# Optimization experiments

Hardware: AMD Instinct MI355X
Metric: run time of the kernel (lower is better)

## Reference

```python
import jax, jax.numpy as jnp
import numpy as np

B, C, IN_LEN, OUT_LEN, E, TOP_K, N_I = 1, 8192, 512, 512, 8, 2, 16


def setup_inputs() -> dict:
    key = jax.random.key(0)
    ks = jax.random.split(key, 8)
    w = lambda k, shape, sc=0.02: jax.random.normal(k, shape, dtype=jnp.float32) * sc
    return {
        "x": jax.random.normal(ks[0], (B, C, IN_LEN), dtype=jnp.float32),
        "Ins_tk": jax.random.normal(ks[1], (B, N_I, OUT_LEN), dtype=jnp.float32),
        "gate_w": w(ks[2], (IN_LEN, E)),            # Gate: Linear(in_len, E, bias=False)
        "expert_w": w(ks[3], (E, IN_LEN, OUT_LEN)),  # per-expert Linear weight (transposed)
        "expert_b": jnp.zeros((E, OUT_LEN), dtype=jnp.float32),
        "gamma_w": w(ks[4], (E, OUT_LEN)),          # EiLM gamma_generator: Linear(h,1,bias=False)
        "beta_w": w(ks[5], (E, OUT_LEN, OUT_LEN)),  # EiLM beta_generator (transposed)
        "rmod_w": w(ks[6], (OUT_LEN, E)),           # router_modulator: Linear(out_len, E, bias=False)
    }


def reference(x, Ins_tk, gate_w, expert_w, expert_b, gamma_w, beta_w, rmod_w):
    Bx, Cx, L = x.shape
    xf = x.reshape(-1, L)                                   # [N, in_len], N = B*C
    ins = Ins_tk[0]                                         # [N_i, out_len] (B==1 asserted)

    # Router: logits + expert-wise modulation of logits
    router_gamma = jnp.mean(ins @ rmod_w, axis=0)           # [E]
    logits = xf @ gate_w + router_gamma                     # [N, E]
    probs = jax.nn.softmax(logits.astype(jnp.float32), axis=-1)
    rw, sel = jax.lax.top_k(probs, TOP_K)                   # [N, k] values/indices (no renorm)

    # Combine weights per token per expert: sum_k rw[t,k] * onehot(sel[t,k])
    combine = jnp.sum(jax.nn.one_hot(sel, E, dtype=rw.dtype) * rw[..., None], axis=1)  # [N, E]

    # EiLM per-expert affine params: scalar gamma, vector beta (mean over instruction tokens)
    gam = jnp.mean(ins @ gamma_w.T, axis=0)                 # [E]
    bet = jnp.einsum('nh,ehd->ed', ins, beta_w) / N_I       # [E, out_len]

    # Per-expert linear over all tokens, then EiLM modulation
    eo = jnp.einsum('nl,eld->end', xf, expert_w) + expert_b[:, None, :]   # [E, N, out]
    mod = gam[:, None, None] * eo + bet[:, None, :]                        # [E, N, out]

    out = jnp.einsum('ne,end->nd', combine, mod)            # [N, out]
    return out.reshape(Bx, Cx, OUT_LEN)
```

## Files before the change

kernel.cpp:

```cpp
#include <hip/hip_runtime.h>
#include <hip/hip_bf16.h>

#define N_TOK 8192
#define INL   512
#define OUTL  512
#define NE    8
#define NI    16
#define EOFF  (OUTL * INL)

typedef unsigned short ushort_t;
typedef unsigned int   uint_t;
typedef short  short8  __attribute__((ext_vector_type(8)));
typedef float  floatx4 __attribute__((ext_vector_type(4)));

#define WS_CNT    0u
#define WS_GAM    4096u
#define WS_RGAM   4352u
#define WS_SCHED  4608u
#define WS_BET    8192u
#define WS_SELW   32768u
#define WS_WT     163840u
#define WS_LIST   4358144u
#define MAXTP     184

__device__ __forceinline__ ushort_t f2bf(float f) {
    uint_t b = __float_as_uint(f);
    return (ushort_t)((b + 0x7FFFu + ((b >> 16) & 1u)) >> 16);
}
__device__ __forceinline__ uint_t pkbf(float a, float b) {
    __hip_bfloat162 h = __float22bfloat162_rn(make_float2(a, b));
    union { __hip_bfloat162 h2; uint_t u; } cv;
    cv.h2 = h;
    return cv.u;
}
__device__ __forceinline__ void dma16(const ushort_t* g, ushort_t* l) {
    __builtin_amdgcn_global_load_lds(
        (const __attribute__((address_space(1))) void*)g,
        (__attribute__((address_space(3))) void*)l,
        16, 0, 0);
}

__global__ __launch_bounds__(256)
void k_prep(const float* __restrict__ ins,
            const float* __restrict__ expert_w,
            const float* __restrict__ expert_b,
            const float* __restrict__ gamma_w,
            const float* __restrict__ beta_w,
            const float* __restrict__ rmod_w,
            ushort_t* __restrict__ wt,
            float* __restrict__ wsBet,
            float* __restrict__ wsGam, float* __restrict__ wsRgam,
            int* __restrict__ wsCnt) {
    __shared__ __align__(16) char smem[17152];
    int bx = blockIdx.x;
    int tid = threadIdx.x;

    if (bx < 512) {
        float (*tile)[65] = (float(*)[65])smem;
        int e = bx >> 6, rem = bx & 63;
        int lt = (rem >> 3) * 64, dt = (rem & 7) * 64;
        int dIdx = tid & 63, lq = tid >> 6;
        for (int i = 0; i < 16; ++i) {
            int l = lq * 16 + i;
            tile[l][dIdx] = expert_w[(e * INL + lt + l) * OUTL + dt + dIdx];
        }
        __syncthreads();
        int lIdx = tid & 63, dq = tid >> 6;
        for (int i = 0; i < 16; ++i) {
            int d = dq * 16 + i;
            wt[(e * OUTL + dt + d) * INL + lt + lIdx] = f2bf(tile[lIdx][d]);
        }
        return;
    }

    if (bx < 640) {
        float* sS  = (float*)smem;
        float* red = sS + 512;
        float* gamS = red + 256;
        int b2 = bx - 512;
        int e = b2 >> 4, dBase = (b2 & 15) * 32;
        for (int h = tid; h < INL; h += 256) {
            float a = 0.f;
            for (int n = 0; n < NI; ++n) a += ins[n * INL + h];
            sS[h] = a;
        }
        __syncthreads();
        if (tid < 64) {
            float g = 0.f;
            for (int j = 0; j < 8; ++j) g += sS[tid * 8 + j] * gamma_w[e * INL + tid * 8 + j];
            for (int off = 32; off >= 1; off >>= 1) g += __shfl_xor(g, off, 64);
            if (tid == 0) gamS[0] = g * (1.f / NI);
        }
        int doff = tid & 31, hq = tid >> 5;
        float a = 0.f;
        for (int j = 0; j < 64; ++j) {
            int h = hq * 64 + j;
            a += sS[h] * beta_w[(e * INL + h) * OUTL + dBase + doff];
        }
        red[tid] = a;
        __syncthreads();
        if (tid < 32) {
            float t = 0.f;
            for (int k = 0; k < 8; ++k) t += red[k * 32 + tid];
            int d = dBase + tid;
            wsBet[e * OUTL + d] = t * (1.f / NI) + gamS[0] * expert_b[e * OUTL + d];
        }
        return;
    }

    {
        if (tid < 64) wsCnt[tid * 16] = 0;
        float* sS = (float*)smem;
        float* pg = sS + 512;
        float* pr = pg + 64;
        for (int h = tid; h < INL; h += 256) {
            float a = 0.f;
            for (int n = 0; n < NI; ++n) a += ins[n * INL + h];
            sS[h] = a;
        }
        __syncthreads();
        if (tid < 64) {
            int e = tid & 7, qq = tid >> 3;
            float g = 0.f, r = 0.f;
            for (int j = 0; j < 64; ++j) {
                int h = qq * 64 + j;
                float sv = sS[h];
                g += sv * gamma_w[e * INL + h];
                r += sv * rmod_w[h * NE + e];
            }
            pg[tid] = g; pr[tid] = r;
        }
        __syncthreads();
        if (tid < NE) {
            float g = 0.f, r = 0.f;
            for (int qq = 0; qq < 8; ++qq) { g += pg[qq * 8 + tid]; r += pr[qq * 8 + tid]; }
            wsGam[tid]  = g * (1.f / NI);
            wsRgam[tid] = r * (1.f / NI);
        }
    }
}

__global__ __launch_bounds__(256)
void k_route(const float* __restrict__ x,
             const float* __restrict__ gate_w,
             const float* __restrict__ wsGam,
             const float* __restrict__ wsRgam,
             float4* __restrict__ selW,
             int* __restrict__ wsCnt, int* __restrict__ wsList) {
    __shared__ float gateT[NE * INL];
    __shared__ int tokP[16];
    __shared__ int cnt64[64], base64[64], pos[16];

    int tid = threadIdx.x;
    for (int i = 0; i < 16; ++i) {
        int f = tid + 256 * i;
        gateT[(f & 7) * INL + (f >> 3)] = gate_w[f];
    }
    if (tid < 64) cnt64[tid] = 0;
    __syncthreads();

    int w = tid >> 6, lane = tid & 63;
    int tbase = blockIdx.x * 16 + w * 4;

    for (int tt = 0; tt < 4; ++tt) {
        int t = tbase + tt;
        float2 xv[4];
        for (int i = 0; i < 4; ++i)
            xv[i] = *(const float2*)(x + (size_t)t * INL + 2 * lane + 128 * i);

        float acc[NE];
        for (int e = 0; e < NE; ++e) acc[e] = 0.f;
        for (int i = 0; i < 4; ++i) {
            int c = 2 * lane + 128 * i;
            for (int e = 0; e < NE; ++e)
                acc[e] += xv[i].x * gateT[e * INL + c] + xv[i].y * gateT[e * INL + c + 1];
        }
        for (int e = 0; e < NE; ++e) {
            float a = acc[e];
            for (int off = 32; off >= 1; off >>= 1) a += __shfl_xor(a, off, 64);
            acc[e] = a;
        }
        float logit[NE];
        for (int e = 0; e < NE; ++e) logit[e] = acc[e] + wsRgam[e];

        int i0 = 0; float m0 = logit[0];
        for (int e = 1; e < NE; ++e) if (logit[e] > m0) { m0 = logit[e]; i0 = e; }
        int i1 = -1; float m1 = -3.4e38f;
        for (int e = 0; e < NE; ++e) if (e != i0 && logit[e] > m1) { m1 = logit[e]; i1 = e; }

        float S = 0.f;
        for (int e = 0; e < NE; ++e) S += expf(logit[e] - m0);
        float rw0 = 1.0f / S;
        float rw1 = expf(m1 - m0) / S;

        if (lane == 0) {
            selW[t] = make_float4(rw0 * wsGam[i0], rw1 * wsGam[i1], rw0, rw1);
            tokP[w * 4 + tt] = i0 * 8 + i1;
        }
    }
    __syncthreads();

    if (tid < 16) pos[tid] = atomicAdd(&cnt64[tokP[tid]], 1);
    __syncthreads();
    if (tid < 64 && cnt64[tid] > 0)
        base64[tid] = atomicAdd(wsCnt + tid * 16, cnt64[tid]);
    __syncthreads();
    if (tid < 16) {
        int p = tokP[tid];
        wsList[(size_t)p * N_TOK + base64[p] + pos[tid]] = blockIdx.x * 16 + tid;
    }
}

__global__ __launch_bounds__(256)
void k_sched(const int* __restrict__ wsCnt, int* __restrict__ sched) {
    __shared__ int cnt[64], base[64], totS;
    int tid = threadIdx.x;
    if (tid < 64) cnt[tid] = wsCnt[tid * 16];
    __syncthreads();
    if (tid == 0) {
        int run = 0;
        for (int i = 0; i < 64; ++i) {
            base[i] = run;
            run += (cnt[i] + 63) >> 6;
        }
        totS = run;
    }
    __syncthreads();
    if (tid < 64) {
        int c = cnt[tid], ti = (c + 63) >> 6, b = base[tid];
        for (int j = 0; j < ti; ++j)
            sched[b + j] = tid | (j << 6) | (c << 14);
    }
    for (int j = totS + tid; j < MAXTP; j += 256)
        sched[j] = -1;
}

__global__ __launch_bounds__(256, 4)
void k_gemmp(const float* __restrict__ x, const ushort_t* __restrict__ wt,
             const int* __restrict__ sched, const int* __restrict__ wsList,
             const float4* __restrict__ selW, const float* __restrict__ wsBet,
             float* __restrict__ out) {
    int bx = blockIdx.x;
    int ct = bx & 7;
    int bt = bx >> 3;

    int s = sched[bt];
    if (s < 0) return;
    int li = s & 63, lt = (s >> 6) & 127, cntE = s >> 14;
    int e0 = li >> 3, e1 = li & 7;
    const int* listE = wsList + (size_t)li * N_TOK;

    __shared__ ushort_t Blds[2][2][64 * 64];

    int tid = threadIdx.x;
    int wid = tid >> 6, lane = tid & 63;
    int wm = wid * 16;
    int mrow = lane & 15, laneq = lane >> 4, q8 = laneq * 8, qr = laneq * 4;

    int idx = lt * 64 + wm + mrow;
    int tok = 0; float w0 = 0.f, w1 = 0.f;
    if (idx < cntE) {
        tok = listE[idx];
        float4 w4 = selW[tok];
        w0 = w4.x; w1 = w4.y;
    }
    const float* arowp = x + (size_t)tok * INL + q8;

    int c0 = tid;
    int col0 = c0 >> 3, kg0 = ((c0 & 7) - col0) & 7;
    const ushort_t* pB = wt + (size_t)e0 * EOFF + (size_t)(ct * 64 + col0) * INL + kg0 * 8;
    ptrdiff_t dE = (ptrdiff_t)(e1 - e0) * EOFF;
    ushort_t* ldsA = &Blds[0][0][0] + wid * 512;

    int fcol[4], frot0[4];
    for (int nt = 0; nt < 4; ++nt) {
        fcol[nt] = nt * 16 + mrow;
        frot0[nt] = (laneq + fcol[nt]) & 7;
    }

    floatx4 comb[4];
    for (int nt = 0; nt < 4; ++nt) comb[nt] = (floatx4){0.f, 0.f, 0.f, 0.f};

    dma16(pB,                 ldsA);
    dma16(pB + 32 * INL,      ldsA + 2048);
    dma16(pB + dE,            ldsA + 4096);
    dma16(pB + dE + 32 * INL, ldsA + 6144);
    float4 a00 = *(const float4*)(arowp);
    float4 a01 = *(const float4*)(arowp + 4);
    float4 a10 = *(const float4*)(arowp + 32);
    float4 a11 = *(const float4*)(arowp + 36);
    __syncthreads();

    #pragma unroll
    for (int kc = 0; kc < 8; ++kc) {
        int buf = kc & 1;
        float4 n00, n01, n10, n11;
        if (kc < 7) {
            const ushort_t* p = pB + (kc + 1) * 64;
            ushort_t* l = ldsA + (buf ^ 1) * 8192;
            dma16(p,                 l);
            dma16(p + 32 * INL,      l + 2048);
            dma16(p + dE,            l + 4096);
            dma16(p + dE + 32 * INL, l + 6144);
            const float* ap = arowp + (kc + 1) * 64;
            n00 = *(const float4*)(ap);
            n01 = *(const float4*)(ap + 4);
            n10 = *(const float4*)(ap + 32);
            n11 = *(const float4*)(ap + 36);
        }

        const ushort_t* Bb = &Blds[buf][0][0];
        #pragma unroll
        for (int e = 0; e < 2; ++e) {
            float wv = e ? w1 : w0;
            union AF { uint4 u; short8 s; } af[2];
            af[0].u.x = pkbf(a00.x * wv, a00.y * wv);
            af[0].u.y = pkbf(a00.z * wv, a00.w * wv);
            af[0].u.z = pkbf(a01.x * wv, a01.y * wv);
            af[0].u.w = pkbf(a01.z * wv, a01.w * wv);
            af[1].u.x = pkbf(a10.x * wv, a10.y * wv);
            af[1].u.y = pkbf(a10.z * wv, a10.w * wv);
            af[1].u.z = pkbf(a11.x * wv, a11.y * wv);
            af[1].u.w = pkbf(a11.z * wv, a11.w * wv);

            const ushort_t* B = Bb + e * 4096;
            short8 bf[4][2];
            #pragma unroll
            for (int nt = 0; nt < 4; ++nt) {
                int cb = fcol[nt] * 64;
                bf[nt][0] = *(const short8*)&B[cb + frot0[nt] * 8];
                bf[nt][1] = *(const short8*)&B[cb + ((frot0[nt] + 4) & 7) * 8];
            }
            #pragma unroll
            for (int ks = 0; ks < 2; ++ks)
                for (int nt = 0; nt < 4; ++nt)
                    comb[nt] = __builtin_amdgcn_mfma_f32_16x16x32_bf16(
                        af[ks].s, bf[nt][ks], comb[nt], 0, 0, 0);
        }
        __syncthreads();
        if (kc < 7) { a00 = n00; a01 = n01; a10 = n10; a11 = n11; }
    }

    #pragma unroll
    for (int ri = 0; ri < 4; ++ri) {
        int idx2 = lt * 64 + wm + qr + ri;
        if (idx2 >= cntE) continue;
        int tok2 = listE[idx2];
        float4 w4 = selW[tok2];
        float* op = out + (size_t)tok2 * OUTL + ct * 64;
        #pragma unroll
        for (int nt = 0; nt < 4; ++nt) {
            int col = ct * 64 + nt * 16 + mrow;
            float bet = w4.z * wsBet[e0 * OUTL + col] + w4.w * wsBet[e1 * OUTL + col];
            op[nt * 16 + mrow] = comb[nt][ri] + bet;
        }
    }
}

extern "C" void kernel_launch(void* const* d_in, const int* in_sizes, int n_in,
                              void* d_out, int out_size, void* d_ws, size_t ws_size,
                              hipStream_t stream) {
    const float* x        = (const float*)d_in[0];
    const float* ins      = (const float*)d_in[1];
    const float* gate_w   = (const float*)d_in[2];
    const float* expert_w = (const float*)d_in[3];
    const float* expert_b = (const float*)d_in[4];
    const float* gamma_w  = (const float*)d_in[5];
    const float* beta_w   = (const float*)d_in[6];
    const float* rmod_w   = (const float*)d_in[7];
    float* out = (float*)d_out;

    char* ws = (char*)d_ws;
    int*      wsCnt  = (int*)(ws + WS_CNT);
    float*    wsGam  = (float*)(ws + WS_GAM);
    float*    wsRgam = (float*)(ws + WS_RGAM);
    int*      wsSch  = (int*)(ws + WS_SCHED);
    float*    wsBet  = (float*)(ws + WS_BET);
    float4*   selW   = (float4*)(ws + WS_SELW);
    ushort_t* wt     = (ushort_t*)(ws + WS_WT);
    int*      wsList = (int*)(ws + WS_LIST);

    k_prep<<<641, 256, 0, stream>>>(ins, expert_w, expert_b,
                                    gamma_w, beta_w, rmod_w,
                                    wt, wsBet, wsGam, wsRgam, wsCnt);
    k_route<<<N_TOK / 16, 256, 0, stream>>>(x, gate_w, wsGam, wsRgam,
                                            selW, wsCnt, wsList);
    k_sched<<<1, 256, 0, stream>>>(wsCnt, wsSch);
    k_gemmp<<<MAXTP * 8, 256, 0, stream>>>(x, wt, wsSch, wsList,
                                           selW, wsBet, out);
}
```

Measured before the change: 139.7 us.

## Double token tile per block to 128 rows, reusing B fragments across two row groups

Each GEMM block now covers 128 tokens instead of 64: every wave handles two 16-row fragments, so each B fragment read from LDS feeds twice as many MFMAs and the expert weight DMA is amortised over more tokens. The schedule splits each expert pair's token list into 128-token tiles, and the grid shrinks to match. The x prefetch into registers is dropped, so A loads now happen inside each k-step, and the k loop is no longer unrolled. This doubles accumulator registers and leaves fewer blocks and more padding waste on partially filled tiles.

```diff
diff --git a/kernel.cpp b/kernel.cpp
--- a/kernel.cpp
+++ b/kernel.cpp
@@ -21,7 +21,7 @@
 #define WS_SELW   32768u
 #define WS_WT     163840u
 #define WS_LIST   4358144u
-#define MAXTP     184
+#define MAXT2     120
 
 __device__ __forceinline__ ushort_t f2bf(float f) {
     uint_t b = __float_as_uint(f);
@@ -221,17 +221,17 @@
         int run = 0;
         for (int i = 0; i < 64; ++i) {
             base[i] = run;
-            run += (cnt[i] + 63) >> 6;
+            run += (cnt[i] + 127) >> 7;
         }
         totS = run;
     }
     __syncthreads();
     if (tid < 64) {
-        int c = cnt[tid], ti = (c + 63) >> 6, b = base[tid];
+        int c = cnt[tid], ti = (c + 127) >> 7, b = base[tid];
         for (int j = 0; j < ti; ++j)
             sched[b + j] = tid | (j << 6) | (c << 14);
     }
-    for (int j = totS + tid; j < MAXTP; j += 256)
+    for (int j = totS + tid; j < MAXT2; j += 256)
         sched[j] = -1;
 }
 
@@ -246,7 +246,7 @@
 
     int s = sched[bt];
     if (s < 0) return;
-    int li = s & 63, lt = (s >> 6) & 127, cntE = s >> 14;
+    int li = s & 63, lt = (s >> 6) & 63, cntE = s >> 14;
     int e0 = li >> 3, e1 = li & 7;
     const int* listE = wsList + (size_t)li * N_TOK;
 
@@ -254,17 +254,23 @@
 
     int tid = threadIdx.x;
     int wid = tid >> 6, lane = tid & 63;
-    int wm = wid * 16;
+    int wm = wid * 32;
     int mrow = lane & 15, laneq = lane >> 4, q8 = laneq * 8, qr = laneq * 4;
 
-    int idx = lt * 64 + wm + mrow;
-    int tok = 0; float w0 = 0.f, w1 = 0.f;
-    if (idx < cntE) {
-        tok = listE[idx];
-        float4 w4 = selW[tok];
-        w0 = w4.x; w1 = w4.y;
-    }
-    const float* arowp = x + (size_t)tok * INL + q8;
+    const float* arowp[2];
+    float w0v[2], w1v[2];
+    #pragma unroll
+    for (int rf = 0; rf < 2; ++rf) {
+        int idx = lt * 128 + wm + rf * 16 + mrow;
+        int tok = 0; float w0 = 0.f, w1 = 0.f;
+        if (idx < cntE) {
+            tok = listE[idx];
+            float4 w4 = selW[tok];
+            w0 = w4.x; w1 = w4.y;
+        }
+        arowp[rf] = x + (size_t)tok * INL + q8;
+        w0v[rf] = w0; w1v[rf] = w1;
+    }
 
     int c0 = tid;
     int col0 = c0 >> 3, kg0 = ((c0 & 7) - col0) & 7;
@@ -278,23 +284,20 @@
         frot0[nt] = (laneq + fcol[nt]) & 7;
     }
 
-    floatx4 comb[4];
-    for (int nt = 0; nt < 4; ++nt) comb[nt] = (floatx4){0.f, 0.f, 0.f, 0.f};
+    floatx4 comb[2][4];
+    #pragma unroll
+    for (int rf = 0; rf < 2; ++rf)
+        for (int nt = 0; nt < 4; ++nt) comb[rf][nt] = (floatx4){0.f, 0.f, 0.f, 0.f};
 
     dma16(pB,                 ldsA);
     dma16(pB + 32 * INL,      ldsA + 2048);
     dma16(pB + dE,            ldsA + 4096);
     dma16(pB + dE + 32 * INL, ldsA + 6144);
-    float4 a00 = *(const float4*)(arowp);
-    float4 a01 = *(const float4*)(arowp + 4);
-    float4 a10 = *(const float4*)(arowp + 32);
-    float4 a11 = *(const float4*)(arowp + 36);
-    __syncthreads();
-
-    #pragma unroll
+    __syncthreads();
+
+    #pragma unroll 1
     for (int kc = 0; kc < 8; ++kc) {
         int buf = kc & 1;
-        float4 n00, n01, n10, n11;
         if (kc < 7) {
             const ushort_t* p = pB + (kc + 1) * 64;
             ushort_t* l = ldsA + (buf ^ 1) * 8192;
@@ -302,27 +305,21 @@
             dma16(p + 32 * INL,      l + 2048);
             dma16(p + dE,            l + 4096);
             dma16(p + dE + 32 * INL, l + 6144);
-            const float* ap = arowp + (kc + 1) * 64;
-            n00 = *(const float4*)(ap);
-            n01 = *(const float4*)(ap + 4);
-            n10 = *(const float4*)(ap + 32);
-            n11 = *(const float4*)(ap + 36);
+        }
+
+        float4 a0[2], a1[2], a2[2], a3[2];
+        #pragma unroll
+        for (int rf = 0; rf < 2; ++rf) {
+            const float* ap = arowp[rf] + kc * 64;
+            a0[rf] = *(const float4*)(ap);
+            a1[rf] = *(const float4*)(ap + 4);
+            a2[rf] = *(const float4*)(ap + 32);
+            a3[rf] = *(const float4*)(ap + 36);
         }
 
         const ushort_t* Bb = &Blds[buf][0][0];
         #pragma unroll
         for (int e = 0; e < 2; ++e) {
-            float wv = e ? w1 : w0;
-            union AF { uint4 u; short8 s; } af[2];
-            af[0].u.x = pkbf(a00.x * wv, a00.y * wv);
-            af[0].u.y = pkbf(a00.z * wv, a00.w * wv);
-            af[0].u.z = pkbf(a01.x * wv, a01.y * wv);
-            af[0].u.w = pkbf(a01.z * wv, a01.w * wv);
-            af[1].u.x = pkbf(a10.x * wv, a10.y * wv);
-            af[1].u.y = pkbf(a10.z * wv, a10.w * wv);
-            af[1].u.z = pkbf(a11.x * wv, a11.y * wv);
-            af[1].u.w = pkbf(a11.z * wv, a11.w * wv);
-
             const ushort_t* B = Bb + e * 4096;
             short8 bf[4][2];
             #pragma unroll
@@ -331,30 +328,44 @@
                 bf[nt][0] = *(const short8*)&B[cb + frot0[nt] * 8];
                 bf[nt][1] = *(const short8*)&B[cb + ((frot0[nt] + 4) & 7) * 8];
             }
+            union AF { uint4 u; short8 s; } af[2][2];
+            #pragma unroll
+            for (int rf = 0; rf < 2; ++rf) {
+                float wv = e ? w1v[rf] : w0v[rf];
+                af[rf][0].u.x = pkbf(a0[rf].x * wv, a0[rf].y * wv);
+                af[rf][0].u.y = pkbf(a0[rf].z * wv, a0[rf].w * wv);
+                af[rf][0].u.z = pkbf(a1[rf].x * wv, a1[rf].y * wv);
+                af[rf][0].u.w = pkbf(a1[rf].z * wv, a1[rf].w * wv);
+                af[rf][1].u.x = pkbf(a2[rf].x * wv, a2[rf].y * wv);
+                af[rf][1].u.y = pkbf(a2[rf].z * wv, a2[rf].w * wv);
+                af[rf][1].u.z = pkbf(a3[rf].x * wv, a3[rf].y * wv);
+                af[rf][1].u.w = pkbf(a3[rf].z * wv, a3[rf].w * wv);
+            }
             #pragma unroll
             for (int ks = 0; ks < 2; ++ks)
-                for (int nt = 0; nt < 4; ++nt)
-                    comb[nt] = __builtin_amdgcn_mfma_f32_16x16x32_bf16(
-                        af[ks].s, bf[nt][ks], comb[nt], 0, 0, 0);
-        }
-        __syncthreads();
-        if (kc < 7) { a00 = n00; a01 = n01; a10 = n10; a11 = n11; }
+                for (int rf = 0; rf < 2; ++rf)
+                    for (int nt = 0; nt < 4; ++nt)
+                        comb[rf][nt] = __builtin_amdgcn_mfma_f32_16x16x32_bf16(
+                            af[rf][ks].s, bf[nt][ks], comb[rf][nt], 0, 0, 0);
+        }
+        __syncthreads();
     }
 
     #pragma unroll
-    for (int ri = 0; ri < 4; ++ri) {
-        int idx2 = lt * 64 + wm + qr + ri;
-        if (idx2 >= cntE) continue;
-        int tok2 = listE[idx2];
-        float4 w4 = selW[tok2];
-        float* op = out + (size_t)tok2 * OUTL + ct * 64;
-        #pragma unroll
-        for (int nt = 0; nt < 4; ++nt) {
-            int col = ct * 64 + nt * 16 + mrow;
-            float bet = w4.z * wsBet[e0 * OUTL + col] + w4.w * wsBet[e1 * OUTL + col];
-            op[nt * 16 + mrow] = comb[nt][ri] + bet;
-        }
-    }
+    for (int rf = 0; rf < 2; ++rf)
+        for (int ri = 0; ri < 4; ++ri) {
+            int idx2 = lt * 128 + wm + rf * 16 + qr + ri;
+            if (idx2 >= cntE) continue;
+            int tok2 = listE[idx2];
+            float4 w4 = selW[tok2];
+            float* op = out + (size_t)tok2 * OUTL + ct * 64;
+            #pragma unroll
+            for (int nt = 0; nt < 4; ++nt) {
+                int col = ct * 64 + nt * 16 + mrow;
+                float bet = w4.z * wsBet[e0 * OUTL + col] + w4.w * wsBet[e1 * OUTL + col];
+                op[nt * 16 + mrow] = comb[rf][nt][ri] + bet;
+            }
+        }
 }
 
 extern "C" void kernel_launch(void* const* d_in, const int* in_sizes, int n_in,
@@ -386,6 +397,6 @@
     k_route<<<N_TOK / 16, 256, 0, stream>>>(x, gate_w, wsGam, wsRgam,
                                             selW, wsCnt, wsList);
     k_sched<<<1, 256, 0, stream>>>(wsCnt, wsSch);
-    k_gemmp<<<MAXTP * 8, 256, 0, stream>>>(x, wt, wsSch, wsList,
+    k_gemmp<<<MAXT2 * 8, 256, 0, stream>>>(x, wt, wsSch, wsList,
                                            selW, wsBet, out);
 }
```

New measurement: 147.9 us. +5.9%, slower.

## Pre-convert x to bf16 in prep and apply routing weights in epilogue

Applied to the files above, without the earlier changes.

Adds extra prep blocks that convert x to bf16 once into workspace. The grouped GEMM then loads bf16 A fragments directly instead of converting and scaling fp32 per expert inside the loop. It keeps two separate accumulators per expert and applies the routing weights in the fp32 epilogue. Block order is also changed so that blocks sharing the same column tile and token tile are adjacent. The cost is more accumulator registers, an extra pass that writes x as bf16, and more prep blocks.

```diff
diff --git a/kernel.cpp b/kernel.cpp
--- a/kernel.cpp
+++ b/kernel.cpp
@@ -21,6 +21,7 @@
 #define WS_SELW   32768u
 #define WS_WT     163840u
 #define WS_LIST   4358144u
+#define WS_XBF    6455296u
 #define MAXTP     184
 
 __device__ __forceinline__ ushort_t f2bf(float f) {
@@ -41,13 +42,15 @@
 }
 
 __global__ __launch_bounds__(256)
-void k_prep(const float* __restrict__ ins,
+void k_prep(const float* __restrict__ x,
+            const float* __restrict__ ins,
             const float* __restrict__ expert_w,
             const float* __restrict__ expert_b,
             const float* __restrict__ gamma_w,
             const float* __restrict__ beta_w,
             const float* __restrict__ rmod_w,
             ushort_t* __restrict__ wt,
+            ushort_t* __restrict__ xbf,
             float* __restrict__ wsBet,
             float* __restrict__ wsGam, float* __restrict__ wsRgam,
             int* __restrict__ wsCnt) {
@@ -108,7 +111,7 @@
         return;
     }
 
-    {
+    if (bx == 640) {
         if (tid < 64) wsCnt[tid * 16] = 0;
         float* sS = (float*)smem;
         float* pg = sS + 512;
@@ -137,6 +140,22 @@
             wsGam[tid]  = g * (1.f / NI);
             wsRgam[tid] = r * (1.f / NI);
         }
+        return;
+    }
+
+    {
+        int b2 = bx - 641;
+        const float* xp = x + (size_t)b2 * 16384;
+        ushort_t* xq = xbf + (size_t)b2 * 16384;
+        #pragma unroll
+        for (int j = 0; j < 16; ++j) {
+            int o = j * 1024 + tid * 4;
+            float4 v = *(const float4*)(xp + o);
+            uint2 u;
+            u.x = pkbf(v.x, v.y);
+            u.y = pkbf(v.z, v.w);
+            *(uint2*)(xq + o) = u;
+        }
     }
 }
 
@@ -236,13 +255,13 @@
 }
 
 __global__ __launch_bounds__(256, 4)
-void k_gemmp(const float* __restrict__ x, const ushort_t* __restrict__ wt,
+void k_gemmp(const ushort_t* __restrict__ xbf, const ushort_t* __restrict__ wt,
              const int* __restrict__ sched, const int* __restrict__ wsList,
              const float4* __restrict__ selW, const float* __restrict__ wsBet,
              float* __restrict__ out) {
     int bx = blockIdx.x;
-    int ct = bx & 7;
-    int bt = bx >> 3;
+    int ct = bx / MAXTP;
+    int bt = bx % MAXTP;
 
     int s = sched[bt];
     if (s < 0) return;
@@ -258,13 +277,9 @@
     int mrow = lane & 15, laneq = lane >> 4, q8 = laneq * 8, qr = laneq * 4;
 
     int idx = lt * 64 + wm + mrow;
-    int tok = 0; float w0 = 0.f, w1 = 0.f;
-    if (idx < cntE) {
-        tok = listE[idx];
-        float4 w4 = selW[tok];
-        w0 = w4.x; w1 = w4.y;
-    }
-    const float* arowp = x + (size_t)tok * INL + q8;
+    int tok = 0;
+    if (idx < cntE) tok = listE[idx];
+    const ushort_t* arowp = xbf + (size_t)tok * INL + q8;
 
     int c0 = tid;
     int col0 = c0 >> 3, kg0 = ((c0 & 7) - col0) & 7;
@@ -278,23 +293,23 @@
         frot0[nt] = (laneq + fcol[nt]) & 7;
     }
 
-    floatx4 comb[4];
-    for (int nt = 0; nt < 4; ++nt) comb[nt] = (floatx4){0.f, 0.f, 0.f, 0.f};
+    floatx4 acc[2][4];
+    #pragma unroll
+    for (int e = 0; e < 2; ++e)
+        for (int nt = 0; nt < 4; ++nt) acc[e][nt] = (floatx4){0.f, 0.f, 0.f, 0.f};
 
     dma16(pB,                 ldsA);
     dma16(pB + 32 * INL,      ldsA + 2048);
     dma16(pB + dE,            ldsA + 4096);
     dma16(pB + dE + 32 * INL, ldsA + 6144);
-    float4 a00 = *(const float4*)(arowp);
-    float4 a01 = *(const float4*)(arowp + 4);
-    float4 a10 = *(const float4*)(arowp + 32);
-    float4 a11 = *(const float4*)(arowp + 36);
+    short8 ca0 = *(const short8*)(arowp);
+    short8 ca1 = *(const short8*)(arowp + 32);
     __syncthreads();
 
     #pragma unroll
     for (int kc = 0; kc < 8; ++kc) {
         int buf = kc & 1;
-        float4 n00, n01, n10, n11;
+        short8 na0, na1;
         if (kc < 7) {
             const ushort_t* p = pB + (kc + 1) * 64;
             ushort_t* l = ldsA + (buf ^ 1) * 8192;
@@ -302,27 +317,14 @@
             dma16(p + 32 * INL,      l + 2048);
             dma16(p + dE,            l + 4096);
             dma16(p + dE + 32 * INL, l + 6144);
-            const float* ap = arowp + (kc + 1) * 64;
-            n00 = *(const float4*)(ap);
-            n01 = *(const float4*)(ap + 4);
-            n10 = *(const float4*)(ap + 32);
-            n11 = *(const float4*)(ap + 36);
+            const ushort_t* ap = arowp + (kc + 1) * 64;
+            na0 = *(const short8*)(ap);
+            na1 = *(const short8*)(ap + 32);
         }
 
         const ushort_t* Bb = &Blds[buf][0][0];
         #pragma unroll
         for (int e = 0; e < 2; ++e) {
-            float wv = e ? w1 : w0;
-            union AF { uint4 u; short8 s; } af[2];
-            af[0].u.x = pkbf(a00.x * wv, a00.y * wv);
-            af[0].u.y = pkbf(a00.z * wv, a00.w * wv);
-            af[0].u.z = pkbf(a01.x * wv, a01.y * wv);
-            af[0].u.w = pkbf(a01.z * wv, a01.w * wv);
-            af[1].u.x = pkbf(a10.x * wv, a10.y * wv);
-            af[1].u.y = pkbf(a10.z * wv, a10.w * wv);
-            af[1].u.z = pkbf(a11.x * wv, a11.y * wv);
-            af[1].u.w = pkbf(a11.z * wv, a11.w * wv);
-
             const ushort_t* B = Bb + e * 4096;
             short8 bf[4][2];
             #pragma unroll
@@ -332,13 +334,15 @@
                 bf[nt][1] = *(const short8*)&B[cb + ((frot0[nt] + 4) & 7) * 8];
             }
             #pragma unroll
-            for (int ks = 0; ks < 2; ++ks)
-                for (int nt = 0; nt < 4; ++nt)
-                    comb[nt] = __builtin_amdgcn_mfma_f32_16x16x32_bf16(
-                        af[ks].s, bf[nt][ks], comb[nt], 0, 0, 0);
-        }
-        __syncthreads();
-        if (kc < 7) { a00 = n00; a01 = n01; a10 = n10; a11 = n11; }
+            for (int nt = 0; nt < 4; ++nt) {
+                acc[e][nt] = __builtin_amdgcn_mfma_f32_16x16x32_bf16(
+                    ca0, bf[nt][0], acc[e][nt], 0, 0, 0);
+                acc[e][nt] = __builtin_amdgcn_mfma_f32_16x16x32_bf16(
+                    ca1, bf[nt][1], acc[e][nt], 0, 0, 0);
+            }
+        }
+        __syncthreads();
+        if (kc < 7) { ca0 = na0; ca1 = na1; }
     }
 
     #pragma unroll
@@ -352,7 +356,7 @@
         for (int nt = 0; nt < 4; ++nt) {
             int col = ct * 64 + nt * 16 + mrow;
             float bet = w4.z * wsBet[e0 * OUTL + col] + w4.w * wsBet[e1 * OUTL + col];
-            op[nt * 16 + mrow] = comb[nt][ri] + bet;
+            op[nt * 16 + mrow] = w4.x * acc[0][nt][ri] + w4.y * acc[1][nt][ri] + bet;
         }
     }
 }
@@ -379,13 +383,14 @@
     float4*   selW   = (float4*)(ws + WS_SELW);
     ushort_t* wt     = (ushort_t*)(ws + WS_WT);
     int*      wsList = (int*)(ws + WS_LIST);
-
-    k_prep<<<641, 256, 0, stream>>>(ins, expert_w, expert_b,
+    ushort_t* xbf    = (ushort_t*)(ws + WS_XBF);
+
+    k_prep<<<897, 256, 0, stream>>>(x, ins, expert_w, expert_b,
                                     gamma_w, beta_w, rmod_w,
-                                    wt, wsBet, wsGam, wsRgam, wsCnt);
+                                    wt, xbf, wsBet, wsGam, wsRgam, wsCnt);
     k_route<<<N_TOK / 16, 256, 0, stream>>>(x, gate_w, wsGam, wsRgam,
                                             selW, wsCnt, wsList);
     k_sched<<<1, 256, 0, stream>>>(wsCnt, wsSch);
-    k_gemmp<<<MAXTP * 8, 256, 0, stream>>>(x, wt, wsSch, wsList,
+    k_gemmp<<<MAXTP * 8, 256, 0, stream>>>(xbf, wt, wsSch, wsList,
                                            selW, wsBet, out);
 }
```

Measured after the change: 130.9 us. 6.3% less time.
